# Kernel optimization log

Measured on AMD Instinct MI355X. Metric: run time of the kernel, lower is better.

The kernel has to match this reference:

```python
import jax, jax.numpy as jnp
import numpy as np

L, B, T, F, C, H, DFF = 2, 4, 2048, 1024, 200, 8, 128


def setup_inputs() -> dict:
    key = jax.random.key(0)
    ks = jax.random.split(key, 12)
    s = 0.02
    return {
        "x": jax.random.normal(ks[0], (B, T, F), jnp.float32),
        "prototypes": jax.random.normal(ks[1], (C, 1, F), jnp.float32),
        # conv_query / conv_key (1x1 convs == linear), per RAB layer
        "wq": jax.random.normal(ks[2], (L, F, F), jnp.float32) * s,
        "bq": jnp.zeros((L, F), jnp.float32),
        "wk": jax.random.normal(ks[3], (L, F, F), jnp.float32) * s,
        "bk": jnp.zeros((L, F), jnp.float32),
        # nn.MultiheadAttention packed in-proj and out-proj
        "in_w": jax.random.normal(ks[4], (L, 3 * F, F), jnp.float32) * s,
        "in_b": jnp.zeros((L, 3 * F), jnp.float32),
        "out_w": jax.random.normal(ks[5], (L, F, F), jnp.float32) * s,
        "out_b": jnp.zeros((L, F), jnp.float32),
        # FFN
        "l1_w": jax.random.normal(ks[6], (L, DFF, F), jnp.float32) * s,
        "l1_b": jnp.zeros((L, DFF), jnp.float32),
        "l2_w": jax.random.normal(ks[7], (L, F, DFF), jnp.float32) * s,
        "l2_b": jnp.zeros((L, F), jnp.float32),
        # LayerNorms
        "ln1_g": jnp.ones((L, F), jnp.float32),
        "ln1_b": jnp.zeros((L, F), jnp.float32),
        "ln2_g": jnp.ones((L, F), jnp.float32),
        "ln2_b": jnp.zeros((L, F), jnp.float32),
        # feature_embedding: Conv1d(F, F, k=3, pad=1) + ReLU
        "emb_w": jax.random.normal(ks[8], (F, F, 3), jnp.float32) * s,
        "emb_b": jnp.zeros((F,), jnp.float32),
    }


def _ln(x, g, b, eps=1e-5):
    mu = jnp.mean(x, axis=-1, keepdims=True)
    var = jnp.mean((x - mu) ** 2, axis=-1, keepdims=True)
    return (x - mu) * jax.lax.rsqrt(var + eps) * g + b


def _mha(q, k, v, w, b, ow, ob):
    # q,k,v: (B,S,F). Packed in-proj like nn.MultiheadAttention (eval: no dropout).
    f = q.shape[-1]
    dh = f // H
    Q = q @ w[:f].T + b[:f]
    K = k @ w[f:2 * f].T + b[f:2 * f]
    V = v @ w[2 * f:].T + b[2 * f:]
    sp = lambda t: t.reshape(t.shape[0], t.shape[1], H, dh)
    scale = np.float32(1.0 / np.sqrt(dh))
    att = jnp.einsum('bqhd,bkhd->bhqk', sp(Q), sp(K)) * scale
    att = jax.nn.softmax(att, axis=-1)
    o = jnp.einsum('bhqk,bkhd->bqhd', att, sp(V)).reshape(q.shape)
    return o @ ow.T + ob


def reference(x, prototypes, wq, bq, wk, bk, in_w, in_b, out_w, out_b,
              l1_w, l1_b, l2_w, l2_b, ln1_g, ln1_b, ln2_g, ln2_b, emb_w, emb_b):
    Bn, Tn, Fn = x.shape
    # torch: prototypes.view(1, F, -1)  (a reshape, NOT a transpose)
    proto = jnp.broadcast_to(prototypes.reshape(1, Fn, -1), (Bn, Fn, prototypes.shape[0]))
    # concat along time: (B,F,S) with S = T + C, then work in (B,S,F)
    src = jnp.swapaxes(jnp.concatenate([jnp.swapaxes(x, 1, 2), proto], axis=2), 1, 2)
    for l in range(L):
        q = src @ wq[l].T + bq[l]          # conv1x1 == pointwise linear
        k = src @ wk[l].T + bk[l]
        a = _mha(q, k, src, in_w[l], in_b[l], out_w[l], out_b[l])
        src = _ln(src + a, ln1_g[l], ln1_b[l])
        ff = jax.nn.relu(src @ l1_w[l].T + l1_b[l]) @ l2_w[l].T + l2_b[l]
        src = _ln(src + ff, ln2_g[l], ln2_b[l])
    feat = jnp.swapaxes(src[:, :Tn], 1, 2)  # (B,F,T): drop prototype tokens
    y = jax.lax.conv_general_dilated(feat, emb_w, (1,), ((1, 1),),
                                     dimension_numbers=('NCH', 'OIH', 'NCH'))
    return jax.nn.relu(y + emb_b[None, :, None])
```

## Files before the change

### kernel.cpp

```cpp
#include <hip/hip_runtime.h>
#include <hip/hip_bf16.h>


constexpr int BN = 4, TN = 2048, FD = 1024, CP = 200, SN = TN + CP;
constexpr int HN = 8, DH = 128, DF = 128, MR = BN * SN;
constexpr int SF = 3 * FD;
constexpr int NT = (SN + 63) / 64;
constexpr float C2 = 0.12751744f;

typedef __attribute__((ext_vector_type(8))) short short8;
typedef __attribute__((ext_vector_type(4))) float f32x4;
typedef __attribute__((ext_vector_type(16))) float f32x16;

__device__ __forceinline__ ushort f2b(float f) {
  union { float f; uint u; } v{f};
  return (ushort)((v.u + 0x7fffu + ((v.u >> 16) & 1u)) >> 16);
}
__device__ __forceinline__ float b2f(ushort u) {
  union { uint u; float f; } v{(uint)u << 16};
  return v.f;
}
__device__ __forceinline__ uint cvt_pk_bf16(float a, float b) {
  uint r;
  asm("v_cvt_pk_bf16_f32 %0, %1, %2" : "=v"(r) : "v"(a), "v"(b));
  return r;
}
__device__ __forceinline__ float exp2_fast(float x) {
  float r;
  asm("v_exp_f32 %0, %1" : "=v"(r) : "v"(x));
  return r;
}
__device__ __forceinline__ void gld16(const void* g, void* l) {
  __builtin_amdgcn_global_load_lds(
      (const __attribute__((address_space(1))) void*)g,
      (__attribute__((address_space(3))) void*)l, 16, 0, 0);
}

__global__ __launch_bounds__(256) void k_build(const float* __restrict__ x,
                                               const float* __restrict__ proto,
                                               ushort* __restrict__ srcb) {
  const int row = blockIdx.x;
  const int b = row / SN, s = row % SN;
  const int f = threadIdx.x * 4;
  const size_t o = (size_t)row * FD + f;
  float4 v;
  if (s < TN) {
    v = *(const float4*)(x + ((size_t)b * TN + s) * FD + f);
  } else {
    const int c = s - TN;
    v.x = proto[(size_t)(f + 0) * CP + c];
    v.y = proto[(size_t)(f + 1) * CP + c];
    v.z = proto[(size_t)(f + 2) * CP + c];
    v.w = proto[(size_t)(f + 3) * CP + c];
  }
  ushort4 u{f2b(v.x), f2b(v.y), f2b(v.z), f2b(v.w)};
  *(ushort4*)(srcb + o) = u;
}

__global__ __launch_bounds__(256) void k_cvt(const float* __restrict__ in,
                                             ushort* __restrict__ out, int n) {
  const int n4 = n >> 2;
  for (int i = blockIdx.x * 256 + threadIdx.x; i < n4; i += gridDim.x * 256) {
    const float4 v = *(const float4*)(in + (size_t)i * 4);
    ushort4 u{f2b(v.x), f2b(v.y), f2b(v.z), f2b(v.w)};
    *(ushort4*)(out + (size_t)i * 4) = u;
  }
}

__global__ __launch_bounds__(256) void k_cvt_inw(const float* __restrict__ in,
                                                 ushort* __restrict__ wInQK,
                                                 ushort* __restrict__ wQKV) {
  constexpr size_t FF = (size_t)FD * FD;
  const int n4 = (int)(6 * FF / 4);
  for (int i = blockIdx.x * 256 + threadIdx.x; i < n4; i += gridDim.x * 256) {
    const size_t idx = (size_t)i * 4;
    const float4 v = *(const float4*)(in + idx);
    ushort4 u{f2b(v.x), f2b(v.y), f2b(v.z), f2b(v.w)};
    const int l = (int)(idx / (3 * FF));
    const size_t r = idx % (3 * FF);
    ushort* dst = (r >= 2 * FF) ? (wQKV + l * 3 * FF + r)
                                : (wInQK + l * 2 * FF + r);
    *(ushort4*)dst = u;
  }
}

__global__ __launch_bounds__(256) void k_cvtT(const float* __restrict__ wq,
                                              const float* __restrict__ wk,
                                              ushort* __restrict__ wT) {
  const int z = blockIdx.z;
  const int qk = z >> 1, l = z & 1;
  const float* W = (qk ? wk : wq) + (size_t)l * FD * FD;
  ushort* WT = wT + (size_t)z * FD * FD;
  __shared__ float t[32][33];
  const int tx = threadIdx.x & 31, ty = threadIdx.x >> 5;
  const int x0 = blockIdx.x * 32, y0 = blockIdx.y * 32;
#pragma unroll
  for (int dy = 0; dy < 4; ++dy)
    t[ty + dy * 8][tx] = W[(size_t)(y0 + ty + dy * 8) * FD + x0 + tx];
  __syncthreads();
#pragma unroll
  for (int dy = 0; dy < 4; ++dy)
    WT[(size_t)(x0 + ty + dy * 8) * FD + y0 + tx] = f2b(t[tx][ty + dy * 8]);
}

__global__ __launch_bounds__(256) void k_vT(const ushort* __restrict__ V,
                                            ushort* __restrict__ Vt) {
  __shared__ ushort t[32][34];
  const int tx = threadIdx.x & 31, ty = threadIdx.x >> 5;
  const int s0 = blockIdx.x * 32, d0 = blockIdx.y * 32, bh = blockIdx.z;
  const int b = bh >> 3, h = bh & 7;
#pragma unroll
  for (int dy = 0; dy < 4; ++dy) {
    const int s = min(s0 + ty + dy * 8, SN - 1);
    t[ty + dy * 8][tx] = V[((size_t)b * SN + s) * SF + h * DH + d0 + tx];
  }
  __syncthreads();
#pragma unroll
  for (int dy = 0; dy < 4; ++dy) {
    const int s = s0 + tx;
    if (s < SN)
      Vt[((size_t)bh * DH + d0 + ty + dy * 8) * SN + s] = t[tx][ty + dy * 8];
  }
}

__global__ __launch_bounds__(256) void k_convw(const float* __restrict__ W,
                                               ushort* __restrict__ out) {
  const int n = FD * FD * 3;
  for (int idx = blockIdx.x * 256 + threadIdx.x; idx < n;
       idx += gridDim.x * 256) {
    const int o = idx / (FD * 3);
    const int rem = idx % (FD * 3);
    const int tau = rem >> 10, i = rem & 1023;
    out[idx] = f2b(W[(size_t)o * (FD * 3) + i * 3 + tau]);
  }
}

__global__ __launch_bounds__(256) void k_pad(const ushort* __restrict__ sb,
                                             ushort* __restrict__ pad) {
  const int r = blockIdx.x, b = blockIdx.y;
  const int f = threadIdx.x * 4;
  ushort4 v{0, 0, 0, 0};
  if (r >= 1 && r <= TN)
    v = *(const ushort4*)(sb + ((size_t)b * SN + (r - 1)) * FD + f);
  *(ushort4*)(pad + ((size_t)b * (TN + 2) + r) * FD + f) = v;
}

__global__ __launch_bounds__(256) void k_beff(const float* __restrict__ in_w,
                                              const float* __restrict__ bq,
                                              const float* __restrict__ bk,
                                              const float* __restrict__ in_b,
                                              float* __restrict__ out) {
  const int n = blockIdx.x, l = blockIdx.y, qk = blockIdx.z;
  const int tid = threadIdx.x;
  if (qk == 2) {
    if (tid == 0)
      out[l * 3 * FD + 2 * FD + n] = in_b[l * 3 * FD + 2 * FD + n];
    return;
  }
  const float* Win = in_w + (size_t)(l * 3 + qk) * FD * FD;
  const float* bv = (qk ? bk : bq) + (size_t)l * FD;
  float s = 0.f;
  for (int j = tid; j < FD; j += 256) s += Win[(size_t)n * FD + j] * bv[j];
  __shared__ float red[4];
#pragma unroll
  for (int o = 32; o; o >>= 1) s += __shfl_xor(s, o);
  if ((tid & 63) == 0) red[tid >> 6] = s;
  __syncthreads();
  if (tid == 0)
    out[l * 3 * FD + qk * FD + n] =
        red[0] + red[1] + red[2] + red[3] + in_b[l * 3 * FD + qk * FD + n];
}

template <bool RELU, bool BF16OUT, bool PREP4 = false>
__global__ __launch_bounds__(256) void k_mm(const ushort* __restrict__ A,
                                            const ushort* __restrict__ W,
                                            const float* __restrict__ bias,
                                            void* __restrict__ Cv,
                                            int M, int N, int K) {
  constexpr size_t FF = (size_t)FD * FD;
  if (PREP4) {
    const int z = blockIdx.z;
    A += (size_t)z * FF;
    W += (size_t)(((z & 1) * 2) + (z >> 1)) * FF;
    Cv = (void*)((ushort*)Cv + (size_t)((z >> 1) * 3 + (z & 1)) * FF);
  }
  __shared__ __align__(16) ushort As[128 * 32];
  __shared__ __align__(16) ushort Ws[128 * 32];
  const int tid = threadIdx.x;
  const int lane = tid & 63, wv = tid >> 6;
  const int l15 = lane & 15, g = lane >> 4;
  const int wr = wv >> 1, wc = wv & 1;
  int bx = blockIdx.x, by = blockIdx.y;
  const int nwg = gridDim.x * gridDim.y;
  if ((nwg & 7) == 0) {
    int bid = by * gridDim.x + bx;
    bid = (bid & 7) * (nwg >> 3) + (bid >> 3);
    bx = bid % gridDim.x;
    by = bid / gridDim.x;
  }
  const int m0 = by * 128, n0 = bx * 128;
  f32x4 acc[4][4];
#pragma unroll
  for (int i = 0; i < 4; ++i)
#pragma unroll
    for (int j = 0; j < 4; ++j) acc[i][j] = (f32x4){0.f, 0.f, 0.f, 0.f};

  for (int k0 = 0; k0 < K; k0 += 32) {
#pragma unroll
    for (int j = 0; j < 2; ++j) {
      const int u = j * 256 + wv * 64 + lane;
      const int r = u >> 2, c = (u & 3) * 8;
      const int gm = min(m0 + r, M - 1);
      gld16(A + (size_t)gm * K + k0 + c, As + (size_t)u * 8);
    }
#pragma unroll
    for (int j = 0; j < 2; ++j) {
      const int u = j * 256 + wv * 64 + lane;
      const int r = u >> 2, c = (u & 3) * 8;
      gld16(W + (size_t)(n0 + r) * K + k0 + c, Ws + (size_t)u * 8);
    }
    __syncthreads();
    short8 af[4], bfr[4];
#pragma unroll
    for (int i = 0; i < 4; ++i)
      af[i] = *(const short8*)(As + (wr * 64 + i * 16 + l15) * 32 + g * 8);
#pragma unroll
    for (int j = 0; j < 4; ++j)
      bfr[j] = *(const short8*)(Ws + (wc * 64 + j * 16 + l15) * 32 + g * 8);
    __builtin_amdgcn_s_setprio(1);
#pragma unroll
    for (int i = 0; i < 4; ++i)
#pragma unroll
      for (int j = 0; j < 4; ++j)
        acc[i][j] = __builtin_amdgcn_mfma_f32_16x16x32_bf16(af[i], bfr[j],
                                                            acc[i][j], 0, 0, 0);
    __builtin_amdgcn_s_setprio(0);
    __syncthreads();
  }
#pragma unroll
  for (int i = 0; i < 4; ++i) {
#pragma unroll
    for (int r = 0; r < 4; ++r) {
      const int row = m0 + wr * 64 + i * 16 + g * 4 + r;
      if (row >= M) continue;
#pragma unroll
      for (int j = 0; j < 4; ++j) {
        const int col = n0 + wc * 64 + j * 16 + l15;
        float v = acc[i][j][r];
        if (bias) v += bias[col];
        if (RELU) v = fmaxf(v, 0.f);
        if (BF16OUT)
          ((ushort*)Cv)[(size_t)row * N + col] = f2b(v);
        else
          ((float*)Cv)[(size_t)row * N + col] = v;
      }
    }
  }
}

template <bool CONV, bool BF16OUT>
__global__ __launch_bounds__(512, 1) void k_mmB(const ushort* __restrict__ A,
                                                const ushort* __restrict__ W,
                                                const float* __restrict__ bias,
                                                void* __restrict__ Cv,
                                                int M, int N, int K) {
  __shared__ __align__(16) ushort As[2][128 * 64];
  __shared__ __align__(16) ushort Bs[2][256 * 64];
  const int tid = threadIdx.x;
  const int lane = tid & 63, wv = tid >> 6;
  const int l15 = lane & 15, g = lane >> 4;
  const int wr = wv >> 2, wc = wv & 3;
  int bx = blockIdx.x, by = blockIdx.y;
  const int nwg = gridDim.x * gridDim.y;
  if ((nwg & 7) == 0) {
    int bid = by * gridDim.x + bx;
    bid = (bid & 7) * (nwg >> 3) + (bid >> 3);
    bx = bid % gridDim.x;
    by = bid / gridDim.x;
  }
  const int m0 = by * 128, n0 = bx * 256;
  const int NKt = K >> 6;

  f32x4 acc[4][4];
#pragma unroll
  for (int i = 0; i < 4; ++i)
#pragma unroll
    for (int j = 0; j < 4; ++j) acc[i][j] = (f32x4){0.f, 0.f, 0.f, 0.f};

  auto stage = [&](int kt, int d) {
    const int kb = kt * 64;
#pragma unroll
    for (int j = 0; j < 2; ++j) {
      const int u = j * 512 + tid;
      const int row = u >> 3, s = u & 7;
      const int c = s ^ (row & 7);
      const ushort* ga;
      if (CONV) {
        const int rm = m0 + row;
        const int bb = rm >> 11, tt = rm & 2047;
        ga = A + (size_t)(bb * (TN + 2) + tt + (kb >> 10)) * FD + (kb & 1023) +
             c * 8;
      } else {
        ga = A + (size_t)min(m0 + row, M - 1) * K + kb + c * 8;
      }
      gld16(ga, As[d] + row * 64 + s * 8);
    }
#pragma unroll
    for (int j = 0; j < 4; ++j) {
      const int u = j * 512 + tid;
      const int row = u >> 3, s = u & 7;
      const int c = s ^ (row & 7);
      gld16(W + (size_t)(n0 + row) * K + kb + c * 8, Bs[d] + row * 64 + s * 8);
    }
  };

  stage(0, 0);
  for (int kt = 0; kt < NKt; ++kt) {
    const int cur = kt & 1;
    if (kt + 1 < NKt) {
      stage(kt + 1, cur ^ 1);
      asm volatile("s_waitcnt vmcnt(6)" ::: "memory");
    } else {
      asm volatile("s_waitcnt vmcnt(0)" ::: "memory");
    }
    __builtin_amdgcn_s_barrier();
    __builtin_amdgcn_sched_barrier(0);
#pragma unroll
    for (int ks = 0; ks < 2; ++ks) {
      short8 aq[4], bq[4];
#pragma unroll
      for (int mf = 0; mf < 4; ++mf) {
        const int row = wr * 64 + mf * 16 + l15;
        aq[mf] = *(const short8*)(As[cur] + row * 64 +
                                  (((ks * 4 + g) ^ (row & 7)) << 3));
      }
#pragma unroll
      for (int nf = 0; nf < 4; ++nf) {
        const int row = wc * 64 + nf * 16 + l15;
        bq[nf] = *(const short8*)(Bs[cur] + row * 64 +
                                  (((ks * 4 + g) ^ (row & 7)) << 3));
      }
      __builtin_amdgcn_s_setprio(1);
#pragma unroll
      for (int mf = 0; mf < 4; ++mf)
#pragma unroll
        for (int nf = 0; nf < 4; ++nf)
          acc[mf][nf] = __builtin_amdgcn_mfma_f32_16x16x32_bf16(
              aq[mf], bq[nf], acc[mf][nf], 0, 0, 0);
      __builtin_amdgcn_s_setprio(0);
    }
    asm volatile("s_waitcnt lgkmcnt(0)" ::: "memory");
    __builtin_amdgcn_s_barrier();
  }

#pragma unroll
  for (int mf = 0; mf < 4; ++mf) {
#pragma unroll
    for (int r = 0; r < 4; ++r) {
      const int row = m0 + wr * 64 + mf * 16 + g * 4 + r;
      if (!CONV && row >= M) continue;
#pragma unroll
      for (int nf = 0; nf < 4; ++nf) {
        const int col = n0 + wc * 64 + nf * 16 + l15;
        float v = acc[mf][nf][r];
        if (bias) v += bias[col];
        if (CONV) {
          v = fmaxf(v, 0.f);
          const int bb = row >> 11, tt = row & 2047;
          ((float*)Cv)[((size_t)(bb * FD + col)) * TN + tt] = v;
        } else if (BF16OUT) {
          ((ushort*)Cv)[(size_t)row * N + col] = f2b(v);
        } else {
          ((float*)Cv)[(size_t)row * N + col] = v;
        }
      }
    }
  }
}

__global__ __launch_bounds__(128) void k_fattn(const ushort* __restrict__ Qg,
                                               const ushort* __restrict__ Kg,
                                               const ushort* __restrict__ Vt,
                                               ushort* __restrict__ Og) {
  __shared__ __align__(16) ushort Ks[64 * 128];
  __shared__ __align__(16) ushort Vs[128 * 64];
  __shared__ __align__(16) ushort Ps[2][32 * 64];
  const int tid = threadIdx.x, lane = tid & 63, wv = tid >> 6;
  const int l31 = lane & 31, hh = lane >> 5;
  const int flat = blockIdx.x + NT * (blockIdx.y + HN * blockIdx.z);
  const int xcd = flat & 7, slot = flat >> 3;
  const int grp = xcd + 8 * (slot / NT);
  const int qt = slot % NT;
  const int b = grp >> 3, h = grp & 7, q0 = qt * 64;
  const size_t rowBase = (size_t)b * SN;
  const int hoff = h * DH;
  const size_t vbase = (size_t)grp * DH * SN;

  short8 qf[8];
  const int qrow = min(q0 + wv * 32 + l31, SN - 1);
#pragma unroll
  for (int ks = 0; ks < 8; ++ks)
    qf[ks] = *(const short8*)(Qg + (rowBase + qrow) * SF + hoff + ks * 16 +
                              hh * 8);

  f32x16 o[4];
#pragma unroll
  for (int dn = 0; dn < 4; ++dn)
#pragma unroll
    for (int r = 0; r < 16; ++r) o[dn][r] = 0.f;
  float lacc = 0.f;
  const char* KsB = (const char*)Ks;
  const char* VsB = (const char*)Vs;
  char* PsB = (char*)&Ps[wv][0];

  for (int t = 0; t < NT; ++t) {
    const int kv0 = t * 64;
    const bool tl = (t == NT - 1);
#pragma unroll
    for (int j = 0; j < 8; ++j) {
      const int su = j * 128 + tid;
      const int row = su >> 4, s = su & 15;
      const int c16 = s ^ (row & 15);
      const int krow = tl ? min(kv0 + row, SN - 1) : kv0 + row;
      gld16(Kg + (rowBase + krow) * SF + hoff + c16 * 8, Ks + (size_t)su * 8);
    }
#pragma unroll
    for (int j = 0; j < 8; ++j) {
      const int su = j * 128 + tid;
      const int row = su >> 3, s = su & 7;
      const int cc = s ^ (row & 7);
      const int kvc = tl ? min(kv0 + cc * 8, SN - 8) : kv0 + cc * 8;
      gld16(Vt + vbase + (size_t)row * SN + kvc, Vs + (size_t)su * 8);
    }
    __syncthreads();

    f32x16 st0, st1;
#pragma unroll
    for (int r = 0; r < 16; ++r) { st0[r] = 0.f; st1[r] = 0.f; }
    __builtin_amdgcn_s_setprio(1);
#pragma unroll
    for (int ks = 0; ks < 8; ++ks) {
      const int slot = (ks * 2 + hh) ^ (l31 & 15);
      const short8 kf0 = *(const short8*)(KsB + l31 * 256 + slot * 16);
      const short8 kf1 = *(const short8*)(KsB + (32 + l31) * 256 + slot * 16);
      st0 = __builtin_amdgcn_mfma_f32_32x32x16_bf16(kf0, qf[ks], st0, 0, 0, 0);
      st1 = __builtin_amdgcn_mfma_f32_32x32x16_bf16(kf1, qf[ks], st1, 0, 0, 0);
    }
    __builtin_amdgcn_s_setprio(0);

    auto smax = [&](const f32x16& stv, int mt) {
      float pfl[16];
      if (tl) {
#pragma unroll
        for (int r = 0; r < 16; ++r) {
          const int kvg = kv0 + mt * 32 + (r & 3) + 8 * (r >> 2) + 4 * hh;
          pfl[r] = (kvg < SN) ? exp2_fast(C2 * stv[r]) : 0.f;
        }
      } else {
#pragma unroll
        for (int r = 0; r < 16; ++r) pfl[r] = exp2_fast(C2 * stv[r]);
      }
      float ls = 0.f;
#pragma unroll
      for (int r = 0; r < 16; ++r) ls += pfl[r];
      lacc += ls;
#pragma unroll
      for (int gg = 0; gg < 4; ++gg) {
        const uint lo = cvt_pk_bf16(pfl[4 * gg + 0], pfl[4 * gg + 1]);
        const uint hi = cvt_pk_bf16(pfl[4 * gg + 2], pfl[4 * gg + 3]);
        const int slot = (mt * 4 + gg) ^ (l31 & 7);
        *(uint2*)(PsB + l31 * 128 + slot * 16 + hh * 8) = make_uint2(lo, hi);
      }
    };
    smax(st0, 0);
    smax(st1, 1);

    __builtin_amdgcn_s_setprio(1);
#pragma unroll
    for (int ks = 0; ks < 4; ++ks) {
      const int pslot = ((ks << 1) | hh) ^ (l31 & 7);
      const short8 pf = *(const short8*)(PsB + l31 * 128 + pslot * 16);
#pragma unroll
      for (int dn = 0; dn < 4; ++dn) {
        const int vrow = dn * 32 + l31;
        const int vslot = ((ks << 1) | hh) ^ (vrow & 7);
        const short8 vf = *(const short8*)(VsB + vrow * 128 + vslot * 16);
        o[dn] = __builtin_amdgcn_mfma_f32_32x32x16_bf16(pf, vf, o[dn], 0, 0, 0);
      }
    }
    __builtin_amdgcn_s_setprio(0);
    __syncthreads();
  }

  lacc += __shfl_xor(lacc, 32);
  const float ir_self = 1.f / lacc;
#pragma unroll
  for (int r = 0; r < 16; ++r) {
    const int ql = (r & 3) + 8 * (r >> 2) + 4 * hh;
    const float ir = __shfl(ir_self, ql);
    const int orow = q0 + wv * 32 + ql;
    if (orow >= SN) continue;
#pragma unroll
    for (int dn = 0; dn < 4; ++dn)
      Og[(rowBase + orow) * FD + hoff + dn * 32 + l31] = f2b(o[dn][r] * ir);
  }
}

__global__ __launch_bounds__(256) void k_add_ln(ushort* __restrict__ sb,
                                                const ushort* __restrict__ d,
                                                const float* __restrict__ g,
                                                const float* __restrict__ be) {
  __shared__ float red[4];
  const int row = blockIdx.x;
  const int tid = threadIdx.x;
  const int c = tid * 4;
  const size_t off = (size_t)row * FD + c;
  const ushort4 sv = *(const ushort4*)(sb + off);
  const ushort4 dv = *(const ushort4*)(d + off);
  float v[4] = {b2f(sv.x) + b2f(dv.x), b2f(sv.y) + b2f(dv.y),
                b2f(sv.z) + b2f(dv.z), b2f(sv.w) + b2f(dv.w)};
  float sum = v[0] + v[1] + v[2] + v[3];
#pragma unroll
  for (int o = 32; o; o >>= 1) sum += __shfl_xor(sum, o);
  if ((tid & 63) == 0) red[tid >> 6] = sum;
  __syncthreads();
  sum = red[0] + red[1] + red[2] + red[3];
  const float mu = sum * (1.f / FD);
  float vs = 0.f;
#pragma unroll
  for (int i = 0; i < 4; ++i) {
    const float t = v[i] - mu;
    vs += t * t;
  }
  __syncthreads();
#pragma unroll
  for (int o = 32; o; o >>= 1) vs += __shfl_xor(vs, o);
  if ((tid & 63) == 0) red[tid >> 6] = vs;
  __syncthreads();
  vs = red[0] + red[1] + red[2] + red[3];
  const float rstd = rsqrtf(vs * (1.f / FD) + 1e-5f);
  const float4 gv = *(const float4*)(g + c);
  const float4 bv = *(const float4*)(be + c);
  ushort4 u{f2b((v[0] - mu) * rstd * gv.x + bv.x),
            f2b((v[1] - mu) * rstd * gv.y + bv.y),
            f2b((v[2] - mu) * rstd * gv.z + bv.z),
            f2b((v[3] - mu) * rstd * gv.w + bv.w)};
  *(ushort4*)(sb + off) = u;
}

extern "C" void kernel_launch(void* const* d_in, const int* in_sizes, int n_in,
                              void* d_out, int out_size, void* d_ws,
                              size_t ws_size, hipStream_t stream) {
  const float* x      = (const float*)d_in[0];
  const float* proto  = (const float*)d_in[1];
  const float* wq     = (const float*)d_in[2];
  const float* bq     = (const float*)d_in[3];
  const float* wk     = (const float*)d_in[4];
  const float* bk     = (const float*)d_in[5];
  const float* in_w   = (const float*)d_in[6];
  const float* in_b   = (const float*)d_in[7];
  const float* out_w  = (const float*)d_in[8];
  const float* out_b  = (const float*)d_in[9];
  const float* l1_w   = (const float*)d_in[10];
  const float* l1_b   = (const float*)d_in[11];
  const float* l2_w   = (const float*)d_in[12];
  const float* l2_b   = (const float*)d_in[13];
  const float* ln1_g  = (const float*)d_in[14];
  const float* ln1_b  = (const float*)d_in[15];
  const float* ln2_g  = (const float*)d_in[16];
  const float* ln2_b  = (const float*)d_in[17];
  const float* emb_w  = (const float*)d_in[18];
  const float* emb_b  = (const float*)d_in[19];

  char* p = (char*)d_ws;
  auto take = [&](size_t bytes) {
    char* r = p;
    p += (bytes + 255) & ~(size_t)255;
    return r;
  };
  const size_t MF = (size_t)MR * FD;
  const size_t FF = (size_t)FD * FD;
  ushort* srcb  = (ushort*)take(MF * 2);
  ushort* bQKV  = (ushort*)take((size_t)MR * SF * 2);
  ushort* bVt   = (ushort*)take((size_t)BN * HN * DH * SN * 2);
  ushort* bO    = (ushort*)take(MF * 2);
  ushort* bFF   = (ushort*)take((size_t)MR * DF * 2);
  ushort* wQKV  = (ushort*)take((size_t)2 * 3 * FF * 2);
  ushort* wOut  = (ushort*)take((size_t)2 * FF * 2);
  ushort* wL1   = (ushort*)take((size_t)2 * DF * FD * 2);
  ushort* wL2   = (ushort*)take((size_t)2 * FD * DF * 2);
  float*  bqkv  = (float*)take((size_t)2 * SF * 4);
  ushort* wT     = bQKV;
  ushort* wInQK  = bQKV + 4 * FF;
  ushort* bOut   = bQKV;
  ushort* srcPad = bQKV;
  ushort* convW  = bQKV + (size_t)10 * 1024 * 1024;

  k_build<<<MR, 256, 0, stream>>>(x, proto, srcb);
  k_cvt_inw<<<2048, 256, 0, stream>>>(in_w, wInQK, wQKV);
  k_cvt<<<1024, 256, 0, stream>>>(out_w, wOut, 2 * FF);
  k_cvt<<<256, 256, 0, stream>>>(l1_w, wL1, 2 * DF * FD);
  k_cvt<<<256, 256, 0, stream>>>(l2_w, wL2, 2 * FD * DF);
  k_cvtT<<<dim3(32, 32, 4), 256, 0, stream>>>(wq, wk, wT);
  k_mm<false, true, true><<<dim3(8, 8, 4), 256, 0, stream>>>(
      wInQK, wT, nullptr, wQKV, FD, FD, FD);
  k_beff<<<dim3(FD, 2, 3), 256, 0, stream>>>(in_w, bq, bk, in_b, bqkv);

  const int MB = (MR + 127) / 128;

  for (int l = 0; l < 2; ++l) {
    k_mmB<false, true><<<dim3(SF / 256, MB), 512, 0, stream>>>(
        srcb, wQKV + (size_t)l * 3 * FF, bqkv + (size_t)l * SF, bQKV, MR, SF,
        FD);
    k_vT<<<dim3((SN + 31) / 32, DH / 32, BN * HN), 256, 0, stream>>>(
        bQKV + 2 * FD, bVt);
    k_fattn<<<dim3(NT, HN, BN), 128, 0, stream>>>(
        bQKV, bQKV + FD, bVt, bO);
    k_mmB<false, true><<<dim3(FD / 256, MB), 512, 0, stream>>>(
        bO, wOut + (size_t)l * FF, out_b + (size_t)l * FD, bOut, MR, FD, FD);
    k_add_ln<<<MR, 256, 0, stream>>>(srcb, bOut, ln1_g + (size_t)l * FD,
                                     ln1_b + (size_t)l * FD);
    k_mm<true, true><<<dim3(DF / 128, MB), 256, 0, stream>>>(
        srcb, wL1 + (size_t)l * DF * FD, l1_b + (size_t)l * DF, bFF, MR, DF,
        FD);
    k_mm<false, true><<<dim3(FD / 128, MB), 256, 0, stream>>>(
        bFF, wL2 + (size_t)l * FD * DF, l2_b + (size_t)l * FD, bOut, MR, FD,
        DF);
    k_add_ln<<<MR, 256, 0, stream>>>(srcb, bOut, ln2_g + (size_t)l * FD,
                                     ln2_b + (size_t)l * FD);
  }

  k_convw<<<1024, 256, 0, stream>>>(emb_w, convW);
  k_pad<<<dim3(TN + 2, BN), 256, 0, stream>>>(srcb, srcPad);
  k_mmB<true, false><<<dim3(FD / 256, (BN * TN) / 128), 512, 0, stream>>>(
      srcPad, convW, emb_b, (float*)d_out, BN * TN, FD, 3 * FD);
}
```

Before: 1.003 ms.

## Split flash-attention KV range in two and combine partials in a separate kernel

The attention kernel now splits the key/value tiles into two halves. Each half runs in its own block and writes an unnormalized bf16 partial output together with its softmax denominator. A new combine kernel adds the two partials and divides by the summed denominators. This doubles the block count, meant to improve CU utilisation and reduce tail imbalance. In exchange it adds an extra pass over the partial buffers plus one more kernel launch, and it rounds the partial sums to bf16 before they are combined.

```diff
diff --git a/kernel.cpp b/kernel.cpp
--- a/kernel.cpp
+++ b/kernel.cpp
@@ -6,6 +6,7 @@
 constexpr int HN = 8, DH = 128, DF = 128, MR = BN * SN;
 constexpr int SF = 3 * FD;
 constexpr int NT = (SN + 63) / 64;
+constexpr int SPLIT = 2, NTH = NT / SPLIT;
 constexpr float C2 = 0.12751744f;
 
 typedef __attribute__((ext_vector_type(8))) short short8;
@@ -381,7 +382,8 @@
 __global__ __launch_bounds__(128) void k_fattn(const ushort* __restrict__ Qg,
                                                const ushort* __restrict__ Kg,
                                                const ushort* __restrict__ Vt,
-                                               ushort* __restrict__ Og) {
+                                               ushort* __restrict__ Op,
+                                               float* __restrict__ lbuf) {
   __shared__ __align__(16) ushort Ks[64 * 128];
   __shared__ __align__(16) ushort Vs[128 * 64];
   __shared__ __align__(16) ushort Ps[2][32 * 64];
@@ -389,12 +391,15 @@
   const int l31 = lane & 31, hh = lane >> 5;
   const int flat = blockIdx.x + NT * (blockIdx.y + HN * blockIdx.z);
   const int xcd = flat & 7, slot = flat >> 3;
-  const int grp = xcd + 8 * (slot / NT);
+  const int c64 = xcd + 8 * (slot / NT);
   const int qt = slot % NT;
-  const int b = grp >> 3, h = grp & 7, q0 = qt * 64;
+  const int h = c64 & 7, z2 = c64 >> 3;
+  const int b = z2 >> 1, sp = z2 & 1;
+  const int q0 = qt * 64;
   const size_t rowBase = (size_t)b * SN;
   const int hoff = h * DH;
-  const size_t vbase = (size_t)grp * DH * SN;
+  const size_t vbase = (size_t)(b * HN + h) * DH * SN;
+  ushort* op = Op + (size_t)sp * MR * FD;
 
   short8 qf[8];
   const int qrow = min(q0 + wv * 32 + l31, SN - 1);
@@ -413,7 +418,7 @@
   const char* VsB = (const char*)Vs;
   char* PsB = (char*)&Ps[wv][0];
 
-  for (int t = 0; t < NT; ++t) {
+  for (int t = sp * NTH; t < sp * NTH + NTH; ++t) {
     const int kv0 = t * 64;
     const bool tl = (t == NT - 1);
 #pragma unroll
@@ -493,17 +498,38 @@
   }
 
   lacc += __shfl_xor(lacc, 32);
-  const float ir_self = 1.f / lacc;
+  const int qself = q0 + wv * 32 + l31;
+  if (hh == 0 && qself < SN)
+    lbuf[((size_t)(sp * BN + b) * HN + h) * SN + qself] = lacc;
 #pragma unroll
   for (int r = 0; r < 16; ++r) {
     const int ql = (r & 3) + 8 * (r >> 2) + 4 * hh;
-    const float ir = __shfl(ir_self, ql);
     const int orow = q0 + wv * 32 + ql;
     if (orow >= SN) continue;
 #pragma unroll
     for (int dn = 0; dn < 4; ++dn)
-      Og[(rowBase + orow) * FD + hoff + dn * 32 + l31] = f2b(o[dn][r] * ir);
-  }
+      op[(rowBase + orow) * FD + hoff + dn * 32 + l31] = f2b(o[dn][r]);
+  }
+}
+
+__global__ __launch_bounds__(256) void k_comb(const ushort* __restrict__ Op,
+                                              const float* __restrict__ lbuf,
+                                              ushort* __restrict__ out) {
+  const int row = blockIdx.x;
+  const int b = row / SN, s = row % SN;
+  const int c = threadIdx.x * 4;
+  const int h = c >> 7;
+  const size_t off = (size_t)row * FD + c;
+  const float l0 = lbuf[((size_t)(0 * BN + b) * HN + h) * SN + s];
+  const float l1 = lbuf[((size_t)(1 * BN + b) * HN + h) * SN + s];
+  const float inv = 1.f / (l0 + l1);
+  const ushort4 a = *(const ushort4*)(Op + off);
+  const ushort4 d = *(const ushort4*)(Op + (size_t)MR * FD + off);
+  ushort4 u{f2b((b2f(a.x) + b2f(d.x)) * inv),
+            f2b((b2f(a.y) + b2f(d.y)) * inv),
+            f2b((b2f(a.z) + b2f(d.z)) * inv),
+            f2b((b2f(a.w) + b2f(d.w)) * inv)};
+  *(ushort4*)(out + off) = u;
 }
 
 __global__ __launch_bounds__(256) void k_add_ln(ushort* __restrict__ sb,
@@ -584,6 +610,8 @@
   ushort* bQKV  = (ushort*)take((size_t)MR * SF * 2);
   ushort* bVt   = (ushort*)take((size_t)BN * HN * DH * SN * 2);
   ushort* bO    = (ushort*)take(MF * 2);
+  ushort* bOp   = (ushort*)take((size_t)SPLIT * MF * 2);
+  float*  lbuf  = (float*)take((size_t)SPLIT * BN * HN * SN * 4);
   ushort* bFF   = (ushort*)take((size_t)MR * DF * 2);
   ushort* wQKV  = (ushort*)take((size_t)2 * 3 * FF * 2);
   ushort* wOut  = (ushort*)take((size_t)2 * FF * 2);
@@ -614,8 +642,9 @@
         FD);
     k_vT<<<dim3((SN + 31) / 32, DH / 32, BN * HN), 256, 0, stream>>>(
         bQKV + 2 * FD, bVt);
-    k_fattn<<<dim3(NT, HN, BN), 128, 0, stream>>>(
-        bQKV, bQKV + FD, bVt, bO);
+    k_fattn<<<dim3(NT, HN, BN * SPLIT), 128, 0, stream>>>(
+        bQKV, bQKV + FD, bVt, bOp, lbuf);
+    k_comb<<<MR, 256, 0, stream>>>(bOp, lbuf, bO);
     k_mmB<false, true><<<dim3(FD / 256, MB), 512, 0, stream>>>(
         bO, wOut + (size_t)l * FF, out_b + (size_t)l * FD, bOut, MR, FD, FD);
     k_add_ln<<<MR, 256, 0, stream>>>(srcb, bOut, ln1_g + (size_t)l * FD,
```

Result: slower. 1.103 ms (+10.0%).
